# Kernel optimization log

Hardware: AMD Instinct MI355X
Metric: run time of the kernel (lower is better)

## Reference

```python
import jax, jax.numpy as jnp
import numpy as np

B, C = 524288, 128


def setup_inputs() -> dict:
    key = jax.random.key(0)
    k1, k2 = jax.random.split(key)
    logit = jax.random.normal(k1, (B, C), dtype=jnp.float32)
    target = jax.random.randint(k2, (B, C), 0, 2, dtype=jnp.int32)
    return {"logit": logit, "target": target}


def _masked_logsumexp(x, mask):
    # logsumexp over entries where mask is True; mask always has >=1 True per row
    neg_big = jnp.finfo(x.dtype).min
    m = jnp.max(jnp.where(mask, x, neg_big), axis=-1, keepdims=True)
    s = jnp.sum(jnp.where(mask, jnp.exp(x - m), 0.0), axis=-1)
    return m[..., 0] + jnp.log(s)


def reference(logit, target):
    t = target.astype(bool)              # [B, C] multi-hot labels
    is_null = t[:, 0]                    # branch 1: null class is active

    # branch 1: -log_softmax(i)[0] over all classes
    lse_all = jax.nn.logsumexp(logit, axis=-1)
    loss_simple = lse_all - logit[:, 0]

    # branch 2a: log-softmax over {0} U positives, mean of -logp over positives
    mask_pos = t.at[:, 0].set(True)
    lse_pos = _masked_logsumexp(logit, mask_pos)
    pos_no0 = t.at[:, 0].set(False)      # positives excluding class 0
    n_pos = pos_no0.sum(axis=-1)
    n_pos_f = n_pos.astype(logit.dtype)
    sum_pos_logit = jnp.sum(jnp.where(pos_no0, logit, 0.0), axis=-1)
    loss_positive = (n_pos_f * lse_pos - sum_pos_logit) / jnp.maximum(n_pos_f, 1.0)

    # branch 2b: log-softmax over negatives (incl. class 0), take class 0
    mask_neg = (~t).at[:, 0].set(True)
    lse_neg = _masked_logsumexp(logit, mask_neg)
    loss_full = loss_positive + lse_neg - logit[:, 0]

    lo = jnp.where(is_null, loss_simple, loss_full)
    return jnp.mean(lo)
```

## Files before the change

### kernel.cpp

```cpp
#include <hip/hip_runtime.h>

#define B_ROWS   524288
#define C_COLS   128
#define THREADS  256
#define BLOCKS   2048
#define NWAVES   (BLOCKS * (THREADS / 64))
#define PAIRS    (B_ROWS / 2)
#define ITERS    (PAIRS / NWAVES)

typedef float f32x4 __attribute__((ext_vector_type(4)));
typedef int   i32x4 __attribute__((ext_vector_type(4)));

template <int CTRL>
__device__ __forceinline__ float dpp_add(float x) {
    union { float f; int i; } u, v;
    u.f = x;
    v.i = __builtin_amdgcn_update_dpp(0, u.i, CTRL, 0xF, 0xF, true);
    return x + v.f;
}

__device__ __forceinline__ float half_wave_reduce(float x) {
    x = dpp_add<0x111>(x);
    x = dpp_add<0x112>(x);
    x = dpp_add<0x114>(x);
    x = dpp_add<0x118>(x);
    x = dpp_add<0x142>(x);
    return x;
}

__device__ __forceinline__ float bcast0_f(float x) {
    union { float f; int i; } u, v;
    u.f = x;
    v.i = __builtin_amdgcn_ds_swizzle(u.i, 0x0000);
    return v.f;
}
__device__ __forceinline__ int bcast0_i(int x) {
    return __builtin_amdgcn_ds_swizzle(x, 0x0000);
}

struct Sums { float s_pos, s_neg, sum_pos, n_pos; };

__device__ __forceinline__ Sums row_sums(f32x4 x, i32x4 t, int l32) {
    Sums s = {0.f, 0.f, 0.f, 0.f};
    {
        const float e  = __expf(x[0]);
        const bool  c0 = (l32 == 0);
        const bool  tt = (t[0] != 0);
        s.s_pos   += (c0 ||  tt) ? e : 0.f;
        s.s_neg   += (c0 || !tt) ? e : 0.f;
        s.n_pos   += (!c0 && tt) ? 1.f  : 0.f;
        s.sum_pos += (!c0 && tt) ? x[0] : 0.f;
    }
    #pragma unroll
    for (int j = 1; j < 4; ++j) {
        const float e = __expf(x[j]);
        const bool tt = (t[j] != 0);
        s.s_pos   += tt ? e : 0.f;
        s.s_neg   += tt ? 0.f : e;
        s.n_pos   += tt ? 1.f : 0.f;
        s.sum_pos += tt ? x[j] : 0.f;
    }
    return s;
}

__device__ __forceinline__ float row_loss(const Sums& s, float x0, int t0) {
    const float e0      = __expf(x0);
    const float s_all   = s.s_pos + s.s_neg - e0;
    const float lse_all = __logf(s_all);
    const float lse_pos = __logf(s.s_pos);
    const float lse_neg = __logf(s.s_neg);
    const float loss_simple   = lse_all - x0;
    const float loss_positive = (s.n_pos * lse_pos - s.sum_pos) / fmaxf(s.n_pos, 1.0f);
    const float loss_full     = loss_positive + lse_neg - x0;
    return t0 ? loss_simple : loss_full;
}

__global__ __launch_bounds__(THREADS) void loss_stage1(
        const float* __restrict__ logit,
        const int*   __restrict__ target,
        float*       __restrict__ partial) {
    const int tid  = blockIdx.x * THREADS + threadIdx.x;
    const int wave = tid >> 6;
    const int lane = threadIdx.x & 63;
    const int half = lane >> 5;
    const int l32  = lane & 31;

    float acc = 0.0f;

    for (int it = 0; it < ITERS / 2; ++it) {
        const int pr0   = wave + (2 * it)     * NWAVES;
        const int pr1   = wave + (2 * it + 1) * NWAVES;
        const int base0 = (pr0 * 2 + half) * C_COLS;
        const int base1 = (pr1 * 2 + half) * C_COLS;

        const f32x4 xa = __builtin_nontemporal_load(
            reinterpret_cast<const f32x4*>(logit  + base0 + l32 * 4));
        const i32x4 ta = __builtin_nontemporal_load(
            reinterpret_cast<const i32x4*>(target + base0 + l32 * 4));
        const f32x4 xb = __builtin_nontemporal_load(
            reinterpret_cast<const f32x4*>(logit  + base1 + l32 * 4));
        const i32x4 tb = __builtin_nontemporal_load(
            reinterpret_cast<const i32x4*>(target + base1 + l32 * 4));

        Sums sa = row_sums(xa, ta, l32);
        Sums sb = row_sums(xb, tb, l32);

        const float x0a = bcast0_f(xa[0]);
        const int   t0a = bcast0_i(ta[0]);
        const float x0b = bcast0_f(xb[0]);
        const int   t0b = bcast0_i(tb[0]);

        sa.s_pos   = half_wave_reduce(sa.s_pos);
        sa.s_neg   = half_wave_reduce(sa.s_neg);
        sa.sum_pos = half_wave_reduce(sa.sum_pos);
        sa.n_pos   = half_wave_reduce(sa.n_pos);
        sb.s_pos   = half_wave_reduce(sb.s_pos);
        sb.s_neg   = half_wave_reduce(sb.s_neg);
        sb.sum_pos = half_wave_reduce(sb.sum_pos);
        sb.n_pos   = half_wave_reduce(sb.n_pos);

        if (l32 == 31) {
            acc += row_loss(sa, x0a, t0a);
            acc += row_loss(sb, x0b, t0b);
        }
    }

    __shared__ float part[2 * (THREADS / 64)];
    const int wlocal = threadIdx.x >> 6;
    if (lane == 31) part[wlocal * 2 + 0] = acc;
    if (lane == 63) part[wlocal * 2 + 1] = acc;
    __syncthreads();
    if (threadIdx.x == 0) {
        float s = 0.f;
        #pragma unroll
        for (int i = 0; i < 2 * (THREADS / 64); ++i) s += part[i];
        partial[blockIdx.x] = s;
    }
}

__global__ __launch_bounds__(256) void loss_stage2(
        const float* __restrict__ partial,
        float*       __restrict__ out) {
    __shared__ float buf[256];
    float s = 0.f;
    for (int i = threadIdx.x; i < BLOCKS; i += 256) s += partial[i];
    buf[threadIdx.x] = s;
    __syncthreads();
    for (int off = 128; off > 0; off >>= 1) {
        if (threadIdx.x < off) buf[threadIdx.x] += buf[threadIdx.x + off];
        __syncthreads();
    }
    if (threadIdx.x == 0) out[0] = buf[0] * (1.0f / (float)B_ROWS);
}

extern "C" void kernel_launch(void* const* d_in, const int* in_sizes, int n_in,
                              void* d_out, int out_size, void* d_ws, size_t ws_size,
                              hipStream_t stream) {
    const float* logit   = (const float*)d_in[0];
    const int*   target  = (const int*)d_in[1];
    float*       out     = (float*)d_out;
    float*       partial = (float*)d_ws;

    loss_stage1<<<BLOCKS, THREADS, 0, stream>>>(logit, target, partial);
    loss_stage2<<<1, 256, 0, stream>>>(partial, out);
}
```

Measured before the change: 92.04 us.

## Software-pipeline loads with contiguous per-wave rows and branchless row sums

The loop now prefetches the next iteration's logit and target vectors before computing the current pair, hiding global load latency behind the exp and reduction work. The row assignment also changes from a grid-strided layout to each wave owning a contiguous block of rows. The per-element masked sums are rewritten using a 0/1 float multiply and fma instead of selects. The cost is doubled register use for the in-flight data, and contiguous per-wave ranges may spread concurrent accesses across DRAM less evenly.

```diff
diff --git a/kernel.cpp b/kernel.cpp
--- a/kernel.cpp
+++ b/kernel.cpp
@@ -7,6 +7,7 @@
 #define NWAVES   (BLOCKS * (THREADS / 64))
 #define PAIRS    (B_ROWS / 2)
 #define ITERS    (PAIRS / NWAVES)
+#define OUTER    (ITERS / 2)
 
 typedef float f32x4 __attribute__((ext_vector_type(4)));
 typedef int   i32x4 __attribute__((ext_vector_type(4)));
@@ -41,24 +42,25 @@
 struct Sums { float s_pos, s_neg, sum_pos, n_pos; };
 
 __device__ __forceinline__ Sums row_sums(f32x4 x, i32x4 t, int l32) {
-    Sums s = {0.f, 0.f, 0.f, 0.f};
+    Sums s;
     {
         const float e  = __expf(x[0]);
         const bool  c0 = (l32 == 0);
         const bool  tt = (t[0] != 0);
-        s.s_pos   += (c0 ||  tt) ? e : 0.f;
-        s.s_neg   += (c0 || !tt) ? e : 0.f;
-        s.n_pos   += (!c0 && tt) ? 1.f  : 0.f;
-        s.sum_pos += (!c0 && tt) ? x[0] : 0.f;
+        s.s_pos   = (c0 ||  tt) ? e : 0.f;
+        s.s_neg   = (c0 || !tt) ? e : 0.f;
+        s.n_pos   = (!c0 && tt) ? 1.f  : 0.f;
+        s.sum_pos = (!c0 && tt) ? x[0] : 0.f;
     }
     #pragma unroll
     for (int j = 1; j < 4; ++j) {
         const float e = __expf(x[j]);
-        const bool tt = (t[j] != 0);
-        s.s_pos   += tt ? e : 0.f;
-        s.s_neg   += tt ? 0.f : e;
-        s.n_pos   += tt ? 1.f : 0.f;
-        s.sum_pos += tt ? x[j] : 0.f;
+        const float f = (t[j] != 0) ? 1.f : 0.f;
+        const float p = f * e;
+        s.s_pos   += p;
+        s.s_neg   += e - p;
+        s.n_pos   += f;
+        s.sum_pos  = fmaf(f, x[j], s.sum_pos);
     }
     return s;
 }
@@ -75,6 +77,44 @@
     return t0 ? loss_simple : loss_full;
 }
 
+__device__ __forceinline__ void load4(const float* __restrict__ logit,
+                                      const int*   __restrict__ target,
+                                      int wave, int half, int l32, int it,
+                                      f32x4& xa, i32x4& ta, f32x4& xb, i32x4& tb) {
+    const int pr0   = wave * ITERS + 2 * it;
+    const int base0 = (pr0 * 2 + half) * C_COLS + l32 * 4;
+    const int base1 = base0 + 2 * C_COLS;
+    xa = __builtin_nontemporal_load(reinterpret_cast<const f32x4*>(logit  + base0));
+    ta = __builtin_nontemporal_load(reinterpret_cast<const i32x4*>(target + base0));
+    xb = __builtin_nontemporal_load(reinterpret_cast<const f32x4*>(logit  + base1));
+    tb = __builtin_nontemporal_load(reinterpret_cast<const i32x4*>(target + base1));
+}
+
+__device__ __forceinline__ void body(f32x4 xa, i32x4 ta, f32x4 xb, i32x4 tb,
+                                     int l32, float& acc) {
+    Sums sa = row_sums(xa, ta, l32);
+    Sums sb = row_sums(xb, tb, l32);
+
+    const float x0a = bcast0_f(xa[0]);
+    const int   t0a = bcast0_i(ta[0]);
+    const float x0b = bcast0_f(xb[0]);
+    const int   t0b = bcast0_i(tb[0]);
+
+    sa.s_pos   = half_wave_reduce(sa.s_pos);
+    sa.s_neg   = half_wave_reduce(sa.s_neg);
+    sa.sum_pos = half_wave_reduce(sa.sum_pos);
+    sa.n_pos   = half_wave_reduce(sa.n_pos);
+    sb.s_pos   = half_wave_reduce(sb.s_pos);
+    sb.s_neg   = half_wave_reduce(sb.s_neg);
+    sb.sum_pos = half_wave_reduce(sb.sum_pos);
+    sb.n_pos   = half_wave_reduce(sb.n_pos);
+
+    if (l32 == 31) {
+        acc += row_loss(sa, x0a, t0a);
+        acc += row_loss(sb, x0b, t0b);
+    }
+}
+
 __global__ __launch_bounds__(THREADS) void loss_stage1(
         const float* __restrict__ logit,
         const int*   __restrict__ target,
@@ -87,43 +127,15 @@
 
     float acc = 0.0f;
 
-    for (int it = 0; it < ITERS / 2; ++it) {
-        const int pr0   = wave + (2 * it)     * NWAVES;
-        const int pr1   = wave + (2 * it + 1) * NWAVES;
-        const int base0 = (pr0 * 2 + half) * C_COLS;
-        const int base1 = (pr1 * 2 + half) * C_COLS;
-
-        const f32x4 xa = __builtin_nontemporal_load(
-            reinterpret_cast<const f32x4*>(logit  + base0 + l32 * 4));
-        const i32x4 ta = __builtin_nontemporal_load(
-            reinterpret_cast<const i32x4*>(target + base0 + l32 * 4));
-        const f32x4 xb = __builtin_nontemporal_load(
-            reinterpret_cast<const f32x4*>(logit  + base1 + l32 * 4));
-        const i32x4 tb = __builtin_nontemporal_load(
-            reinterpret_cast<const i32x4*>(target + base1 + l32 * 4));
-
-        Sums sa = row_sums(xa, ta, l32);
-        Sums sb = row_sums(xb, tb, l32);
-
-        const float x0a = bcast0_f(xa[0]);
-        const int   t0a = bcast0_i(ta[0]);
-        const float x0b = bcast0_f(xb[0]);
-        const int   t0b = bcast0_i(tb[0]);
-
-        sa.s_pos   = half_wave_reduce(sa.s_pos);
-        sa.s_neg   = half_wave_reduce(sa.s_neg);
-        sa.sum_pos = half_wave_reduce(sa.sum_pos);
-        sa.n_pos   = half_wave_reduce(sa.n_pos);
-        sb.s_pos   = half_wave_reduce(sb.s_pos);
-        sb.s_neg   = half_wave_reduce(sb.s_neg);
-        sb.sum_pos = half_wave_reduce(sb.sum_pos);
-        sb.n_pos   = half_wave_reduce(sb.n_pos);
-
-        if (l32 == 31) {
-            acc += row_loss(sa, x0a, t0a);
-            acc += row_loss(sb, x0b, t0b);
-        }
+    f32x4 xa, xb; i32x4 ta, tb;
+    load4(logit, target, wave, half, l32, 0, xa, ta, xb, tb);
+    for (int it = 0; it < OUTER - 1; ++it) {
+        f32x4 nxa, nxb; i32x4 nta, ntb;
+        load4(logit, target, wave, half, l32, it + 1, nxa, nta, nxb, ntb);
+        body(xa, ta, xb, tb, l32, acc);
+        xa = nxa; ta = nta; xb = nxb; tb = ntb;
     }
+    body(xa, ta, xb, tb, l32, acc);
 
     __shared__ float part[2 * (THREADS / 64)];
     const int wlocal = threadIdx.x >> 6;
```

After: 89.70 us, median of 2. 2.5% less time.
